# Optimization experiments

Hardware: AMD Instinct MI355X
Metric: run time of the kernel (lower is better)

## Reference

```python
import jax, jax.numpy as jnp
import numpy as np

# Fixed B3-spline 5-tap weights (non-trainable in the torch module)
W5 = jnp.array([1/16, 1/4, 3/8, 1/4, 1/16], dtype=jnp.float32)
LEVEL = 3  # J
DIM = 2    # spatial dims (H, W)


def _conv1d_reflect(y, axis, dil):
    """5-tap dilated conv along `axis` with reflect padding of 2*dil (same size).

    Matches torch Conv1d(1,1,5, dilation=dil, padding=2*dil, padding_mode='reflect').
    """
    p = 2 * dil
    pads = [(0, 0)] * y.ndim
    pads[axis] = (p, p)
    yp = jnp.pad(y, pads, mode='reflect')  # torch 'reflect' == jnp 'reflect'
    L = y.shape[axis]
    out = W5[0] * jax.lax.slice_in_dim(yp, 0, L, axis=axis)
    for k in range(1, 5):
        out = out + W5[k] * jax.lax.slice_in_dim(yp, k * dil, k * dil + L, axis=axis)
    return out


def setup_inputs() -> dict:
    key = jax.random.key(0)
    x = jax.random.normal(key, (16, 1024, 1024), dtype=jnp.float32)  # (B, H, W)
    return {"x": x}


def reference(x):
    # x: (B, H, W); returns (B, LEVEL+1, H, W) = [w_1, ..., w_J, c_J]
    y = x
    details = []
    for j in range(LEVEL):
        prev = y
        dil = 2 ** j
        for axis in range(1, 1 + DIM):  # spatial axes of (B, H, W)
            y = _conv1d_reflect(y, axis, dil)
        details.append(prev - y)  # w_{j+1}
    return jnp.stack(details + [y], axis=1)
```

## Files before the change

### kernel.cpp

```cpp
#include <hip/hip_runtime.h>


#define HH 1024
#define WW 1024
#define STRIDE 256
#define EMITW 224
#define HSEG 64
#define NCH (HSEG / 8 + 4)

typedef unsigned short u16;
typedef unsigned int u32;
typedef float f4 __attribute__((ext_vector_type(4)));

__device__ __forceinline__ int reflect_i(int g, int n) {
    if (g < 0) g = -g;
    else if (g >= n) g = 2 * n - 2 - g;
    return g;
}
__device__ __forceinline__ float bl(u32 u) { return __uint_as_float(u << 16); }
__device__ __forceinline__ float bh(u32 u) { return __uint_as_float(u & 0xffff0000u); }
__device__ __forceinline__ u32 pack2(float a, float b) {
    u32 ua = __float_as_uint(a); ua += 0x7fff + ((ua >> 16) & 1);
    u32 ub = __float_as_uint(b); ub += 0x7fff + ((ub >> 16) & 1);
    return (ua >> 16) | (ub & 0xffff0000u);
}
__device__ __forceinline__ void unpack8(uint4 v, float* f) {
    f[0] = bl(v.x); f[1] = bh(v.x);
    f[2] = bl(v.y); f[3] = bh(v.y);
    f[4] = bl(v.z); f[5] = bh(v.z);
    f[6] = bl(v.w); f[7] = bh(v.w);
}
__device__ constexpr float K0 = 1.0f / 16.0f;
__device__ constexpr float K1 = 4.0f / 16.0f;
__device__ constexpr float K2 = 6.0f / 16.0f;

__device__ __forceinline__ int rslot(int q) { return (q + 128) & 31; }

template <int D>
__device__ __forceinline__ void conv_vh(const u16* __restrict__ src, int q, int c8,
                                        int lane, float* h) {
    uint4 tv[5];
#pragma unroll
    for (int k = 0; k < 5; ++k)
        tv[k] = *(const uint4*)(src + rslot(q + (k - 2) * D) * STRIDE + 8 * c8);
    float v8[8];
    {
        float a[8], b[8];
        unpack8(tv[0], a); unpack8(tv[4], b);
#pragma unroll
        for (int c = 0; c < 8; ++c) v8[c] = K0 * (a[c] + b[c]);
        unpack8(tv[1], a); unpack8(tv[3], b);
#pragma unroll
        for (int c = 0; c < 8; ++c) v8[c] += K1 * (a[c] + b[c]);
        unpack8(tv[2], a);
#pragma unroll
        for (int c = 0; c < 8; ++c) v8[c] += K2 * a[c];
    }
    float ext[8 + 4 * D];
#pragma unroll
    for (int c = 0; c < 8; ++c) ext[2 * D + c] = v8[c];
#pragma unroll
    for (int j = 0; j < 2 * D; ++j) {
        ext[j]             = __shfl(v8[8 - 2 * D + j], lane - 1);
        ext[2 * D + 8 + j] = __shfl(v8[j], lane + 1);
    }
#pragma unroll
    for (int c = 0; c < 8; ++c)
        h[c] = K0 * (ext[c] + ext[c + 4 * D]) + K1 * (ext[c + D] + ext[c + 3 * D])
             + K2 * ext[c + 2 * D];
}

__device__ __forceinline__ void ring_write(u16* dst, int q, int c8, const float* h) {
    uint4 ov;
    ov.x = pack2(h[0], h[1]); ov.y = pack2(h[2], h[3]);
    ov.z = pack2(h[4], h[5]); ov.w = pack2(h[6], h[7]);
    *(uint4*)(dst + rslot(q) * STRIDE + 8 * c8) = ov;
}

__device__ __forceinline__ void nt4(float* p, float a, float b, float c, float d) {
    f4 v; v.x = a; v.y = b; v.z = c; v.w = d;
    __builtin_nontemporal_store(v, (f4*)p);
}

__global__ __launch_bounds__(256, 3) void uwt3_stream(const float* __restrict__ x,
                                                      float* __restrict__ out) {
    __shared__ __align__(16) u16 ring[3][32][STRIDE];
    u16* xr  = &ring[0][0][0];
    u16* y1r = &ring[1][0][0];
    u16* y2r = &ring[2][0][0];
    const int tid = threadIdx.x;
    const int lane = tid & 63;
    const int rowic = 2 * (tid >> 6) + (lane >> 5);
    const int c8 = lane & 31;
    const int stripe0 = blockIdx.x * EMITW;
    const int R0 = blockIdx.y * HSEG;
    const int bz = blockIdx.z;
    const float* xb = x + (size_t)bz * HH * WW;
    const size_t PL = (size_t)HH * WW;

    for (int t = 0; t < NCH; ++t) {
        const int r = R0 - 32 + 8 * t;

        {
            int q = r + 14 + rowic;
            int gr = reflect_i(q, HH);
            int w0 = stripe0 - 16 + 8 * c8;
            const float* row = xb + (size_t)gr * WW;
            float f[8];
            if (w0 >= 0 && w0 + 7 < WW) {
                float4 a = *(const float4*)(row + w0);
                float4 b = *(const float4*)(row + w0 + 4);
                f[0] = a.x; f[1] = a.y; f[2] = a.z; f[3] = a.w;
                f[4] = b.x; f[5] = b.y; f[6] = b.z; f[7] = b.w;
            } else {
#pragma unroll
                for (int k = 0; k < 8; ++k) f[k] = row[reflect_i(w0 + k, WW)];
            }
            uint4 v;
            v.x = pack2(f[0], f[1]); v.y = pack2(f[2], f[3]);
            v.z = pack2(f[4], f[5]); v.w = pack2(f[6], f[7]);
            *(uint4*)(xr + rslot(q) * STRIDE + 8 * c8) = v;
        }
        __syncthreads();

        if (t >= 1) {
            float h[8];
            int q = r + 12 + rowic;
            conv_vh<1>(xr, q, c8, lane, h);
            ring_write(y1r, q, c8, h);
        }
        __syncthreads();

        if (t >= 2) {
            float h[8];
            int q = r + 8 + rowic;
            conv_vh<2>(y1r, q, c8, lane, h);
            ring_write(y2r, q, c8, h);
        }
        __syncthreads();

        if (t >= 4) {
            int q = r + rowic;
            float h[8];
            conv_vh<4>(y2r, q, c8, lane, h);
            if (c8 >= 2 && c8 < 30) {
                int w = stripe0 + 8 * c8 - 16;
                if (w < WW) {
                    float xv[8], a1[8], a2[8];
                    const int so = rslot(q) * STRIDE + 8 * c8;
                    unpack8(*(const uint4*)(xr + so), xv);
                    unpack8(*(const uint4*)(y1r + so), a1);
                    unpack8(*(const uint4*)(y2r + so), a2);
                    size_t b0 = (((size_t)bz * 4) * HH + q) * (size_t)WW + w;
                    nt4(out + b0,              xv[0]-a1[0], xv[1]-a1[1], xv[2]-a1[2], xv[3]-a1[3]);
                    nt4(out + b0 + 4,          xv[4]-a1[4], xv[5]-a1[5], xv[6]-a1[6], xv[7]-a1[7]);
                    nt4(out + b0 + PL,         a1[0]-a2[0], a1[1]-a2[1], a1[2]-a2[2], a1[3]-a2[3]);
                    nt4(out + b0 + PL + 4,     a1[4]-a2[4], a1[5]-a2[5], a1[6]-a2[6], a1[7]-a2[7]);
                    nt4(out + b0 + 2*PL,       a2[0]-h[0],  a2[1]-h[1],  a2[2]-h[2],  a2[3]-h[3]);
                    nt4(out + b0 + 2*PL + 4,   a2[4]-h[4],  a2[5]-h[5],  a2[6]-h[6],  a2[7]-h[7]);
                    nt4(out + b0 + 3*PL,       h[0], h[1], h[2], h[3]);
                    nt4(out + b0 + 3*PL + 4,   h[4], h[5], h[6], h[7]);
                }
            }
        }
    }
}

extern "C" void kernel_launch(void* const* d_in, const int* in_sizes, int n_in,
                              void* d_out, int out_size, void* d_ws, size_t ws_size,
                              hipStream_t stream) {
    const float* x = (const float*)d_in[0];
    float* out = (float*)d_out;
    dim3 grid((WW + EMITW - 1) / EMITW, HH / HSEG, 16);
    uwt3_stream<<<grid, dim3(256, 1, 1), 0, stream>>>(x, out);
}
```

Before: 373.8 us.

## Prefetch input rows into registers, shrink rings, emit details per stage

```diff
diff --git a/kernel.cpp b/kernel.cpp
--- a/kernel.cpp
+++ b/kernel.cpp
@@ -6,11 +6,11 @@
 #define STRIDE 256
 #define EMITW 224
 #define HSEG 64
-#define NCH (HSEG / 8 + 4)
+#define NCH 13
 
 typedef unsigned short u16;
 typedef unsigned int u32;
-typedef float f4 __attribute__((ext_vector_type(4)));
+typedef float f4v __attribute__((ext_vector_type(4)));
 
 __device__ __forceinline__ int reflect_i(int g, int n) {
     if (g < 0) g = -g;
@@ -34,15 +34,15 @@
 __device__ constexpr float K1 = 4.0f / 16.0f;
 __device__ constexpr float K2 = 6.0f / 16.0f;
 
-__device__ __forceinline__ int rslot(int q) { return (q + 128) & 31; }
-
-template <int D>
+template <int D, int RMASK>
 __device__ __forceinline__ void conv_vh(const u16* __restrict__ src, int q, int c8,
-                                        int lane, float* h) {
+                                        int lane, float* h, float* ctr) {
     uint4 tv[5];
 #pragma unroll
-    for (int k = 0; k < 5; ++k)
-        tv[k] = *(const uint4*)(src + rslot(q + (k - 2) * D) * STRIDE + 8 * c8);
+    for (int k = 0; k < 5; ++k) {
+        int s = (q + (k - 2) * D + 256) & RMASK;
+        tv[k] = *(const uint4*)(src + s * STRIDE + 8 * c8);
+    }
     float v8[8];
     {
         float a[8], b[8];
@@ -52,9 +52,9 @@
         unpack8(tv[1], a); unpack8(tv[3], b);
 #pragma unroll
         for (int c = 0; c < 8; ++c) v8[c] += K1 * (a[c] + b[c]);
-        unpack8(tv[2], a);
+        unpack8(tv[2], ctr);
 #pragma unroll
-        for (int c = 0; c < 8; ++c) v8[c] += K2 * a[c];
+        for (int c = 0; c < 8; ++c) v8[c] += K2 * ctr[c];
     }
     float ext[8 + 4 * D];
 #pragma unroll
@@ -70,24 +70,41 @@
              + K2 * ext[c + 2 * D];
 }
 
-__device__ __forceinline__ void ring_write(u16* dst, int q, int c8, const float* h) {
+__device__ __forceinline__ void ring_write(u16* dst, int slot, int c8, const float* h) {
     uint4 ov;
     ov.x = pack2(h[0], h[1]); ov.y = pack2(h[2], h[3]);
     ov.z = pack2(h[4], h[5]); ov.w = pack2(h[6], h[7]);
-    *(uint4*)(dst + rslot(q) * STRIDE + 8 * c8) = ov;
+    *(uint4*)(dst + slot * STRIDE + 8 * c8) = ov;
 }
 
-__device__ __forceinline__ void nt4(float* p, float a, float b, float c, float d) {
-    f4 v; v.x = a; v.y = b; v.z = c; v.w = d;
-    __builtin_nontemporal_store(v, (f4*)p);
+__device__ __forceinline__ void emit2(float* __restrict__ out, size_t base,
+                                      const float* a) {
+    f4v v0; v0.x = a[0]; v0.y = a[1]; v0.z = a[2]; v0.w = a[3];
+    f4v v1; v1.x = a[4]; v1.y = a[5]; v1.z = a[6]; v1.w = a[7];
+    __builtin_nontemporal_store(v0, (f4v*)(out + base));
+    __builtin_nontemporal_store(v1, (f4v*)(out + base + 4));
 }
 
-__global__ __launch_bounds__(256, 3) void uwt3_stream(const float* __restrict__ x,
-                                                      float* __restrict__ out) {
-    __shared__ __align__(16) u16 ring[3][32][STRIDE];
-    u16* xr  = &ring[0][0][0];
-    u16* y1r = &ring[1][0][0];
-    u16* y2r = &ring[2][0][0];
+__device__ __forceinline__ void load_row(const float* __restrict__ xb, int q,
+                                         int w0, float* f) {
+    int gr = reflect_i(q, HH);
+    const float* row = xb + (size_t)gr * WW;
+    if (w0 >= 0 && w0 + 7 < WW) {
+        float4 a = *(const float4*)(row + w0);
+        float4 b = *(const float4*)(row + w0 + 4);
+        f[0] = a.x; f[1] = a.y; f[2] = a.z; f[3] = a.w;
+        f[4] = b.x; f[5] = b.y; f[6] = b.z; f[7] = b.w;
+    } else {
+#pragma unroll
+        for (int k = 0; k < 8; ++k) f[k] = row[reflect_i(w0 + k, WW)];
+    }
+}
+
+__global__ __launch_bounds__(256, 4) void uwt3_stream2(const float* __restrict__ x,
+                                                       float* __restrict__ out) {
+    __shared__ __align__(16) u16 xr[16 * STRIDE];
+    __shared__ __align__(16) u16 y1r[16 * STRIDE];
+    __shared__ __align__(16) u16 y2r[32 * STRIDE];
     const int tid = threadIdx.x;
     const int lane = tid & 63;
     const int rowic = 2 * (tid >> 6) + (lane >> 5);
@@ -97,70 +114,64 @@
     const int bz = blockIdx.z;
     const float* xb = x + (size_t)bz * HH * WW;
     const size_t PL = (size_t)HH * WW;
+    const int w0 = stripe0 - 16 + 8 * c8;
+    const bool colok = (c8 >= 2 && c8 < 30 && w0 < WW);
+    const size_t ob = ((size_t)bz * 4) * PL + w0;
+
+    float xf[8];
+    load_row(xb, R0 - 32 + 14 + rowic, w0, xf);
 
     for (int t = 0; t < NCH; ++t) {
         const int r = R0 - 32 + 8 * t;
 
-        {
+        if (t <= 11) {
             int q = r + 14 + rowic;
-            int gr = reflect_i(q, HH);
-            int w0 = stripe0 - 16 + 8 * c8;
-            const float* row = xb + (size_t)gr * WW;
-            float f[8];
-            if (w0 >= 0 && w0 + 7 < WW) {
-                float4 a = *(const float4*)(row + w0);
-                float4 b = *(const float4*)(row + w0 + 4);
-                f[0] = a.x; f[1] = a.y; f[2] = a.z; f[3] = a.w;
-                f[4] = b.x; f[5] = b.y; f[6] = b.z; f[7] = b.w;
-            } else {
-#pragma unroll
-                for (int k = 0; k < 8; ++k) f[k] = row[reflect_i(w0 + k, WW)];
-            }
             uint4 v;
-            v.x = pack2(f[0], f[1]); v.y = pack2(f[2], f[3]);
-            v.z = pack2(f[4], f[5]); v.w = pack2(f[6], f[7]);
-            *(uint4*)(xr + rslot(q) * STRIDE + 8 * c8) = v;
+            v.x = pack2(xf[0], xf[1]); v.y = pack2(xf[2], xf[3]);
+            v.z = pack2(xf[4], xf[5]); v.w = pack2(xf[6], xf[7]);
+            *(uint4*)(xr + ((q + 256) & 15) * STRIDE + 8 * c8) = v;
         }
         __syncthreads();
 
-        if (t >= 1) {
-            float h[8];
+        if (t <= 10)
+            load_row(xb, r + 22 + rowic, w0, xf);
+
+        if (t >= 1 && t <= 11) {
             int q = r + 12 + rowic;
-            conv_vh<1>(xr, q, c8, lane, h);
-            ring_write(y1r, q, c8, h);
+            float h[8], ctr[8];
+            conv_vh<1, 15>(xr, q, c8, lane, h, ctr);
+            ring_write(y1r, (q + 256) & 15, c8, h);
+            if (colok && (unsigned)(q - R0) < HSEG) {
+                float d[8];
+#pragma unroll
+                for (int i = 0; i < 8; ++i) d[i] = ctr[i] - h[i];
+                emit2(out, ob + (size_t)q * WW, d);
+            }
         }
         __syncthreads();
 
-        if (t >= 2) {
-            float h[8];
+        if (t >= 2 && t <= 11) {
             int q = r + 8 + rowic;
-            conv_vh<2>(y1r, q, c8, lane, h);
-            ring_write(y2r, q, c8, h);
+            float h[8], ctr[8];
+            conv_vh<2, 15>(y1r, q, c8, lane, h, ctr);
+            ring_write(y2r, (q + 256) & 31, c8, h);
+            if (colok && (unsigned)(q - R0) < HSEG) {
+                float d[8];
+#pragma unroll
+                for (int i = 0; i < 8; ++i) d[i] = ctr[i] - h[i];
+                emit2(out, ob + PL + (size_t)q * WW, d);
+            }
         }
-        __syncthreads();
-
-        if (t >= 4) {
-            int q = r + rowic;
-            float h[8];
-            conv_vh<4>(y2r, q, c8, lane, h);
-            if (c8 >= 2 && c8 < 30) {
-                int w = stripe0 + 8 * c8 - 16;
-                if (w < WW) {
-                    float xv[8], a1[8], a2[8];
-                    const int so = rslot(q) * STRIDE + 8 * c8;
-                    unpack8(*(const uint4*)(xr + so), xv);
-                    unpack8(*(const uint4*)(y1r + so), a1);
-                    unpack8(*(const uint4*)(y2r + so), a2);
-                    size_t b0 = (((size_t)bz * 4) * HH + q) * (size_t)WW + w;
-                    nt4(out + b0,              xv[0]-a1[0], xv[1]-a1[1], xv[2]-a1[2], xv[3]-a1[3]);
-                    nt4(out + b0 + 4,          xv[4]-a1[4], xv[5]-a1[5], xv[6]-a1[6], xv[7]-a1[7]);
-                    nt4(out + b0 + PL,         a1[0]-a2[0], a1[1]-a2[1], a1[2]-a2[2], a1[3]-a2[3]);
-                    nt4(out + b0 + PL + 4,     a1[4]-a2[4], a1[5]-a2[5], a1[6]-a2[6], a1[7]-a2[7]);
-                    nt4(out + b0 + 2*PL,       a2[0]-h[0],  a2[1]-h[1],  a2[2]-h[2],  a2[3]-h[3]);
-                    nt4(out + b0 + 2*PL + 4,   a2[4]-h[4],  a2[5]-h[5],  a2[6]-h[6],  a2[7]-h[7]);
-                    nt4(out + b0 + 3*PL,       h[0], h[1], h[2], h[3]);
-                    nt4(out + b0 + 3*PL + 4,   h[4], h[5], h[6], h[7]);
-                }
+        if (t >= 5) {
+            int q = r - 8 + rowic;
+            float h[8], ctr[8];
+            conv_vh<4, 31>(y2r, q, c8, lane, h, ctr);
+            if (colok && (unsigned)(q - R0) < HSEG) {
+                float d[8];
+#pragma unroll
+                for (int i = 0; i < 8; ++i) d[i] = ctr[i] - h[i];
+                emit2(out, ob + 2 * PL + (size_t)q * WW, d);
+                emit2(out, ob + 3 * PL + (size_t)q * WW, h);
             }
         }
     }
@@ -172,5 +183,5 @@
     const float* x = (const float*)d_in[0];
     float* out = (float*)d_out;
     dim3 grid((WW + EMITW - 1) / EMITW, HH / HSEG, 16);
-    uwt3_stream<<<grid, dim3(256, 1, 1), 0, stream>>>(x, out);
+    uwt3_stream2<<<grid, dim3(256, 1, 1), 0, stream>>>(x, out);
 }
```

After: 347.8 us. -6.9%, faster.
